# Optimization experiments

Measured on AMD Instinct MI355X. Metric: run time of the kernel, lower is better.

The kernel has to match this reference:

```python
import jax, jax.numpy as jnp
import numpy as np

EPS_NORM = 1e-12  # F.normalize eps
EPS_BN = 1e-5     # BatchNorm1d eps


def _gather_neighbors(tensor, index):
    # tensor: (bs, v, d), index: (bs, v, n) -> (bs, v, n, d)
    return jax.vmap(lambda t, i: t[i])(tensor, index)


def setup_inputs() -> dict:
    key = jax.random.key(0)
    ks = jax.random.split(key, 8)
    bs, v, n = 4, 4096, 32
    cin, cout = 128, 256
    stdv = float(np.sqrt(2.0 / cout))
    return {
        "neighbor_index": jax.random.randint(ks[0], (bs, v, n), 0, v),
        "vertices": jax.random.normal(ks[1], (bs, v, 3), dtype=jnp.float32),
        "feature_map": jax.random.normal(ks[2], (bs, v, cin - 1), dtype=jnp.float32),
        "directions": jax.random.uniform(ks[3], (4, cout), minval=-stdv, maxval=stdv, dtype=jnp.float32),
        "W": jax.random.normal(ks[4], (cout, cin), dtype=jnp.float32) / np.sqrt(cin),
        "b": jnp.zeros((cout,), jnp.float32),
        "gamma": jnp.ones((cout,), jnp.float32),
        "beta": jnp.zeros((cout,), jnp.float32),
    }


def reference(neighbor_index, vertices, feature_map, directions, W, b, gamma, beta):
    # --- direction-based weights theta: (bs, v, n, cout) ---
    neighbors = _gather_neighbors(vertices, neighbor_index)          # (bs,v,n,3)
    direc = neighbors - vertices[:, :, None, :]
    direc_norm = direc / jnp.maximum(
        jnp.linalg.norm(direc, axis=-1, keepdims=True), EPS_NORM)    # F.normalize
    dir_w = (direc_norm + 1.0) * 0.5                                  # (bs,v,n,3)
    sup_w = jnp.stack([directions[1] - directions[0],
                       directions[2] - directions[0],
                       directions[3] - directions[0]], axis=0)        # (3, cout)
    theta = jax.nn.relu(jnp.einsum('bvnk,kc->bvnc', dir_w, sup_w) + directions[0])

    # --- gathered features + L2 distance channel ---
    fs = _gather_neighbors(feature_map, neighbor_index)               # (bs,v,n,cin-1)
    fdist = jnp.sqrt(jnp.sum(fs * fs, axis=-1, keepdims=True))        # (bs,v,n,1)
    fs = jnp.concatenate([fs, fdist], axis=-1)                        # (bs,v,n,cin)

    # --- Linear -> BatchNorm1d (training stats) -> ReLU ---
    z = jnp.einsum('bvni,ci->bvnc', fs, W) + b                        # (bs,v,n,cout)
    mean = jnp.mean(z, axis=(0, 1, 2))
    var = jnp.mean(jnp.square(z - mean), axis=(0, 1, 2))              # biased var
    zn = (z - mean) * jax.lax.rsqrt(var + EPS_BN) * gamma + beta
    act = jax.nn.relu(zn) * theta

    # --- max-pool over neighbor dim ---
    return jnp.max(act, axis=2)                                       # (bs,v,cout)
```

## Files before the change

### kernel.cpp

```cpp
#include <hip/hip_runtime.h>

typedef unsigned short ushort_t;
typedef __attribute__((ext_vector_type(8))) short short8;
typedef __attribute__((ext_vector_type(4))) float floatx4;
typedef __attribute__((ext_vector_type(2))) float floatx2;

#define NN    32
#define CIN   128
#define COUT  256
#define NPTS  16384
#define NSAMP (NPTS * NN)
#define LDA   136
#define HB    128

__device__ __align__(16) ushort_t g_wb[COUT * CIN];
__device__ __align__(16) ushort_t g_y[(size_t)NPTS * COUT];
__device__ __align__(16) int      g_hp[HB * 4096];
__device__ __align__(16) float    g_sp[256 * 512];
__device__ __align__(16) float    g_consts[1536];

__device__ __forceinline__ float bf2f(ushort_t u) {
    return __uint_as_float(((unsigned int)u) << 16);
}
__device__ __forceinline__ ushort_t f2bf(float f) {
    unsigned int x = __float_as_uint(f);
    return (ushort_t)((x + 0x7FFFu + ((x >> 16) & 1u)) >> 16);
}
__device__ __forceinline__ int probe_f32(const void* verts, int lane) {
    float ax = fabsf(bf2f(((const ushort_t*)verts)[lane]));
    unsigned long long b = __ballot((ax > 1e-5f) && (ax < 32.0f));
    return (__popcll(b) >= 56) ? 0 : 1;
}

__global__ __launch_bounds__(256)
void hist_kernel(const int* __restrict__ nbr,
                 const void* __restrict__ Wg,
                 const void* __restrict__ verts) {
    __shared__ int h[4096];
    const int b   = blockIdx.x;
    const int tid = threadIdx.x;
    if (b < HB) {
        #pragma unroll
        for (int i = 0; i < 16; ++i) h[i * 256 + tid] = 0;
        __syncthreads();
        const int* src = nbr + (size_t)b * 4096;
        #pragma unroll
        for (int i = 0; i < 16; ++i) atomicAdd(&h[src[i * 256 + tid]], 1);
        __syncthreads();
        int* dst = g_hp + (size_t)b * 4096;
        #pragma unroll
        for (int i = 0; i < 16; ++i) dst[i * 256 + tid] = h[i * 256 + tid];
    } else {
        const int f32 = probe_f32(verts, tid & 63);
        int i = (b - HB) * 1024 + tid * 4;
        if (f32) {
            float4 v = ((const float4*)Wg)[i >> 2];
            g_wb[i] = f2bf(v.x); g_wb[i + 1] = f2bf(v.y);
            g_wb[i + 2] = f2bf(v.z); g_wb[i + 3] = f2bf(v.w);
        } else {
            *(uint2*)(g_wb + i) = *(const uint2*)((const ushort_t*)Wg + i);
        }
    }
}

__global__ __launch_bounds__(256, 2)
void ygemm_kernel(const void* __restrict__ fm, const void* __restrict__ verts) {
    __shared__ __align__(16) ushort_t At[64 * LDA];
    __shared__ float multS[64];

    const int tid  = threadIdx.x;
    const int r0   = blockIdx.x * 64;
    const int lane = tid & 63;
    const int f32  = probe_f32(verts, lane);

    if (tid < 64) {
        const int* hp = g_hp + (size_t)(r0 >> 12) * 32 * 4096 + (r0 & 4095) + tid;
        int s = 0;
        #pragma unroll
        for (int p2 = 0; p2 < 32; ++p2) s += hp[(size_t)p2 * 4096];
        multS[tid] = (float)s;
    }

    const int rl4 = tid >> 6;
    #pragma unroll 4
    for (int i = 0; i < 16; ++i) {
        const int rl = i * 4 + rl4;
        float f0, f1; ushort_t u0, u1;
        if (f32) {
            const float* src = (const float*)fm + (size_t)(r0 + rl) * 127;
            f0 = src[lane];
            f1 = (lane < 63) ? src[64 + lane] : 0.0f;
            u0 = f2bf(f0); u1 = f2bf(f1);
        } else {
            const ushort_t* src = (const ushort_t*)fm + (size_t)(r0 + rl) * 127;
            u0 = src[lane];
            u1 = (lane < 63) ? src[64 + lane] : (ushort_t)0;
            f0 = bf2f(u0); f1 = bf2f(u1);
        }
        float ss = f0 * f0 + f1 * f1;
        #pragma unroll
        for (int d = 1; d < 64; d <<= 1) ss += __shfl_xor(ss, d, 64);
        At[rl * LDA + lane]      = u0;
        At[rl * LDA + 64 + lane] = (lane < 63) ? u1 : f2bf(sqrtf(ss));
    }
    __syncthreads();

    const int w = tid >> 6;
    const int m = lane & 15;
    const int q = lane >> 4;

    floatx4 acc[4][4];
    #pragma unroll
    for (int rt = 0; rt < 4; ++rt)
        #pragma unroll
        for (int ct = 0; ct < 4; ++ct)
            acc[rt][ct] = (floatx4){0.0f, 0.0f, 0.0f, 0.0f};

    #pragma unroll
    for (int kk = 0; kk < 4; ++kk) {
        const int kof = kk * 32 + q * 8;
        short8 af[4];
        #pragma unroll
        for (int rt = 0; rt < 4; ++rt)
            af[rt] = *(const short8*)&At[(rt * 16 + m) * LDA + kof];
        short8 bfr[4];
        #pragma unroll
        for (int ct = 0; ct < 4; ++ct) {
            int ch = w * 64 + ct * 16 + m;
            bfr[ct] = *(const short8*)(g_wb + ch * CIN + kof);
        }
        #pragma unroll
        for (int rt = 0; rt < 4; ++rt)
            #pragma unroll
            for (int ct = 0; ct < 4; ++ct)
                acc[rt][ct] = __builtin_amdgcn_mfma_f32_16x16x32_bf16(
                    af[rt], bfr[ct], acc[rt][ct], 0, 0, 0);
    }

    #pragma unroll
    for (int ct = 0; ct < 4; ++ct) {
        const int ch = w * 64 + ct * 16 + m;
        float s = 0.0f, ss = 0.0f;
        #pragma unroll
        for (int rt = 0; rt < 4; ++rt)
            #pragma unroll
            for (int j = 0; j < 4; ++j) {
                int rloc = rt * 16 + q * 4 + j;
                ushort_t yb = f2bf(acc[rt][ct][j]);
                g_y[(size_t)(r0 + rloc) * COUT + ch] = yb;
                float yv = bf2f(yb);
                float wm = multS[rloc];
                s  += wm * yv;
                ss += wm * yv * yv;
            }
        s  += __shfl_xor(s, 16, 64);  s  += __shfl_xor(s, 32, 64);
        ss += __shfl_xor(ss, 16, 64); ss += __shfl_xor(ss, 32, 64);
        if (q == 0) {
            g_sp[(size_t)blockIdx.x * 512 + ch]       = s;
            g_sp[(size_t)blockIdx.x * 512 + 256 + ch] = ss;
        }
    }
}

__global__ void finalize_kernel(const void* __restrict__ gamma,
                                const void* __restrict__ beta,
                                const void* __restrict__ dirs,
                                const void* __restrict__ verts) {
    const int c   = threadIdx.x;
    const int f32 = probe_f32(verts, c & 63);

    float s = 0.0f, ss = 0.0f;
    #pragma unroll 8
    for (int p2 = 0; p2 < 256; ++p2) {
        s  += g_sp[(size_t)p2 * 512 + c];
        ss += g_sp[(size_t)p2 * 512 + 256 + c];
    }
    const float invN = 1.0f / (float)NSAMP;
    float mean = s * invN;
    float var  = fmaxf(ss * invN - mean * mean, 0.0f);
    float inv  = 1.0f / sqrtf(var + 1e-5f);
    float ga, be, d0, d1, d2, d3;
    if (f32) {
        ga = ((const float*)gamma)[c]; be = ((const float*)beta)[c];
        const float* dd = (const float*)dirs;
        d0 = dd[c]; d1 = dd[256 + c]; d2 = dd[512 + c]; d3 = dd[768 + c];
    } else {
        ga = bf2f(((const ushort_t*)gamma)[c]); be = bf2f(((const ushort_t*)beta)[c]);
        const ushort_t* dd = (const ushort_t*)dirs;
        d0 = bf2f(dd[c]); d1 = bf2f(dd[256 + c]);
        d2 = bf2f(dd[512 + c]); d3 = bf2f(dd[768 + c]);
    }
    float scale = ga * inv;
    g_consts[c]        = scale;
    g_consts[256 + c]  = be - mean * scale;
    g_consts[512 + c]  = d0;
    g_consts[768 + c]  = d1 - d0;
    g_consts[1024 + c] = d2 - d0;
    g_consts[1280 + c] = d3 - d0;
}

__global__ __launch_bounds__(256, 4)
void epi_kernel(const int* __restrict__ nbr,
                const void* __restrict__ verts,
                void* __restrict__ out) {
    __shared__ float4 dws[4][NN];

    const int tid  = threadIdx.x;
    const int lane = tid & 63;
    const int bid  = blockIdx.x;
    const int p0   = (((bid & 7) << 9) | (bid >> 3)) << 2;
    const int f32  = probe_f32(verts, lane);

    if (tid < 128) {
        const int pt = tid >> 5, j = tid & 31;
        const int p  = p0 + pt;
        int gv = ((p >> 12) << 12) + nbr[(size_t)p * NN + j];
        float sx, sy, sz, nx, ny, nz;
        if (f32) {
            const float* vv = (const float*)verts;
            sx = vv[p * 3]; sy = vv[p * 3 + 1]; sz = vv[p * 3 + 2];
            nx = vv[gv * 3]; ny = vv[gv * 3 + 1]; nz = vv[gv * 3 + 2];
        } else {
            const ushort_t* vv = (const ushort_t*)verts;
            sx = bf2f(vv[p * 3]); sy = bf2f(vv[p * 3 + 1]); sz = bf2f(vv[p * 3 + 2]);
            nx = bf2f(vv[gv * 3]); ny = bf2f(vv[gv * 3 + 1]); nz = bf2f(vv[gv * 3 + 2]);
        }
        float dx = nx - sx, dy = ny - sy, dz = nz - sz;
        float nrm = sqrtf(dx * dx + dy * dy + dz * dz);
        float inv = 1.0f / fmaxf(nrm, 1e-12f);
        dws[pt][j] = make_float4((dx * inv + 1.0f) * 0.5f,
                                 (dy * inv + 1.0f) * 0.5f,
                                 (dz * inv + 1.0f) * 0.5f,
                                 __int_as_float(gv));
    }
    __syncthreads();

    const int w  = tid >> 6;
    const int p  = p0 + w;
    const int c4 = lane * 4;
    const floatx4 zero = {0.0f, 0.0f, 0.0f, 0.0f};
    const floatx4 sc = *(const floatx4*)&g_consts[c4];
    const floatx4 sh = *(const floatx4*)&g_consts[256 + c4];
    const floatx4 d0 = *(const floatx4*)&g_consts[512 + c4];
    const floatx4 s0 = *(const floatx4*)&g_consts[768 + c4];
    const floatx4 s1 = *(const floatx4*)&g_consts[1024 + c4];
    const floatx4 s2 = *(const floatx4*)&g_consts[1280 + c4];

    const float4* dwp = dws[w];
    floatx4 vmA = zero, vmB = zero;

    for (int j0 = 0; j0 < NN; j0 += 4) {
        float4 dw[4]; uint2 u[4];
        #pragma unroll
        for (int jj = 0; jj < 4; ++jj) {
            dw[jj] = dwp[j0 + jj];
            int row = __float_as_int(dw[jj].w);
            u[jj] = *(const uint2*)(g_y + ((size_t)row << 8) + c4);
        }
        #pragma unroll
        for (int jj = 0; jj < 4; ++jj) {
            floatx4 y;
            y.x = __uint_as_float(u[jj].x << 16);
            y.y = __uint_as_float(u[jj].x & 0xFFFF0000u);
            y.z = __uint_as_float(u[jj].y << 16);
            y.w = __uint_as_float(u[jj].y & 0xFFFF0000u);
            floatx4 th = d0 + s0 * dw[jj].x + s1 * dw[jj].y + s2 * dw[jj].z;
            th = __builtin_elementwise_max(th, zero);
            floatx4 zt = (y * sc + sh) * th;
            if (jj & 1) vmB = __builtin_elementwise_max(vmB, zt);
            else        vmA = __builtin_elementwise_max(vmA, zt);
        }
    }
    floatx4 vm = __builtin_elementwise_max(vmA, vmB);

    size_t ofs = (size_t)p * COUT + c4;
    if (f32) {
        *(floatx4*)((float*)out + ofs) = vm;
    } else {
        uint2 ou;
        ou.x = ((unsigned int)f2bf(vm.y) << 16) | (unsigned int)f2bf(vm.x);
        ou.y = ((unsigned int)f2bf(vm.w) << 16) | (unsigned int)f2bf(vm.z);
        *(uint2*)((ushort_t*)out + ofs) = ou;
    }
}

extern "C" void kernel_launch(void* const* d_in, const int* in_sizes, int n_in,
                              void* d_out, int out_size, void* d_ws, size_t ws_size,
                              hipStream_t stream) {
    const int* nbr    = (const int*)d_in[0];
    const void* verts = d_in[1];
    const void* fm    = d_in[2];
    const void* dirs  = d_in[3];
    const void* Wg    = d_in[4];
    const void* gamma = d_in[6];
    const void* beta  = d_in[7];
    (void)d_ws; (void)ws_size; (void)in_sizes; (void)n_in; (void)out_size;

    hist_kernel<<<dim3(HB + 32), dim3(256), 0, stream>>>(nbr, Wg, verts);
    ygemm_kernel<<<dim3(NPTS / 64), dim3(256), 0, stream>>>(fm, verts);
    finalize_kernel<<<dim3(1), dim3(256), 0, stream>>>(gamma, beta, dirs, verts);
    epi_kernel<<<dim3(NPTS / 4), dim3(256), 0, stream>>>(nbr, verts, d_out);
}
```

Before: 141.0 us.

## Use per-wave readlane broadcasts and 8-deep load pipeline in epilogue

Each wave now computes its own point's neighbor direction weights in registers, lanes 0-31 holding one neighbor each, and broadcasts them with readlane. This removes the shared-memory staging and the block barrier. The gather of bf16 rows from the intermediate buffer is software-pipelined eight loads deep instead of four, and launch bounds rise to five blocks per SM. Each wave does the direction computation redundantly in its upper 32 lanes, and the deeper prefetch raises register pressure against the higher occupancy target.

```diff
diff --git a/kernel.cpp b/kernel.cpp
--- a/kernel.cpp
+++ b/kernel.cpp
@@ -30,6 +30,9 @@
     float ax = fabsf(bf2f(((const ushort_t*)verts)[lane]));
     unsigned long long b = __ballot((ax > 1e-5f) && (ax < 32.0f));
     return (__popcll(b) >= 56) ? 0 : 1;
+}
+__device__ __forceinline__ float lanebcast(float v, int jj) {
+    return __uint_as_float((unsigned)__builtin_amdgcn_readlane(__float_as_int(v), jj));
 }
 
 __global__ __launch_bounds__(256)
@@ -199,22 +202,22 @@
     g_consts[1280 + c] = d3 - d0;
 }
 
-__global__ __launch_bounds__(256, 4)
+__global__ __launch_bounds__(256, 5)
 void epi_kernel(const int* __restrict__ nbr,
                 const void* __restrict__ verts,
                 void* __restrict__ out) {
-    __shared__ float4 dws[4][NN];
-
     const int tid  = threadIdx.x;
     const int lane = tid & 63;
     const int bid  = blockIdx.x;
     const int p0   = (((bid & 7) << 9) | (bid >> 3)) << 2;
+    const int p    = p0 + (tid >> 6);
     const int f32  = probe_f32(verts, lane);
-
-    if (tid < 128) {
-        const int pt = tid >> 5, j = tid & 31;
-        const int p  = p0 + pt;
-        int gv = ((p >> 12) << 12) + nbr[(size_t)p * NN + j];
+    const int j    = lane & 31;
+
+    int   gv;
+    float wx, wy, wz;
+    {
+        gv = ((p >> 12) << 12) + nbr[(size_t)p * NN + j];
         float sx, sy, sz, nx, ny, nz;
         if (f32) {
             const float* vv = (const float*)verts;
@@ -228,15 +231,11 @@
         float dx = nx - sx, dy = ny - sy, dz = nz - sz;
         float nrm = sqrtf(dx * dx + dy * dy + dz * dz);
         float inv = 1.0f / fmaxf(nrm, 1e-12f);
-        dws[pt][j] = make_float4((dx * inv + 1.0f) * 0.5f,
-                                 (dy * inv + 1.0f) * 0.5f,
-                                 (dz * inv + 1.0f) * 0.5f,
-                                 __int_as_float(gv));
-    }
-    __syncthreads();
-
-    const int w  = tid >> 6;
-    const int p  = p0 + w;
+        wx = (dx * inv + 1.0f) * 0.5f;
+        wy = (dy * inv + 1.0f) * 0.5f;
+        wz = (dz * inv + 1.0f) * 0.5f;
+    }
+
     const int c4 = lane * 4;
     const floatx4 zero = {0.0f, 0.0f, 0.0f, 0.0f};
     const floatx4 sc = *(const floatx4*)&g_consts[c4];
@@ -246,29 +245,37 @@
     const floatx4 s1 = *(const floatx4*)&g_consts[1024 + c4];
     const floatx4 s2 = *(const floatx4*)&g_consts[1280 + c4];
 
-    const float4* dwp = dws[w];
     floatx4 vmA = zero, vmB = zero;
-
-    for (int j0 = 0; j0 < NN; j0 += 4) {
-        float4 dw[4]; uint2 u[4];
-        #pragma unroll
-        for (int jj = 0; jj < 4; ++jj) {
-            dw[jj] = dwp[j0 + jj];
-            int row = __float_as_int(dw[jj].w);
-            u[jj] = *(const uint2*)(g_y + ((size_t)row << 8) + c4);
-        }
-        #pragma unroll
-        for (int jj = 0; jj < 4; ++jj) {
+    uint2 u[8];
+
+    #pragma unroll
+    for (int k = 0; k < 8; ++k) {
+        int r = __builtin_amdgcn_readlane(gv, k);
+        u[k] = *(const uint2*)(g_y + ((size_t)(unsigned)r << 8) + c4);
+    }
+    #pragma unroll
+    for (int g = 0; g < 4; ++g) {
+        #pragma unroll
+        for (int k = 0; k < 8; ++k) {
+            const int jj = g * 8 + k;
+            const uint2 uk = u[k];
+            if (g < 3) {
+                int r = __builtin_amdgcn_readlane(gv, jj + 8);
+                u[k] = *(const uint2*)(g_y + ((size_t)(unsigned)r << 8) + c4);
+            }
+            float wxs = lanebcast(wx, jj);
+            float wys = lanebcast(wy, jj);
+            float wzs = lanebcast(wz, jj);
             floatx4 y;
-            y.x = __uint_as_float(u[jj].x << 16);
-            y.y = __uint_as_float(u[jj].x & 0xFFFF0000u);
-            y.z = __uint_as_float(u[jj].y << 16);
-            y.w = __uint_as_float(u[jj].y & 0xFFFF0000u);
-            floatx4 th = d0 + s0 * dw[jj].x + s1 * dw[jj].y + s2 * dw[jj].z;
+            y.x = __uint_as_float(uk.x << 16);
+            y.y = __uint_as_float(uk.x & 0xFFFF0000u);
+            y.z = __uint_as_float(uk.y << 16);
+            y.w = __uint_as_float(uk.y & 0xFFFF0000u);
+            floatx4 th = d0 + s0 * wxs + s1 * wys + s2 * wzs;
             th = __builtin_elementwise_max(th, zero);
             floatx4 zt = (y * sc + sh) * th;
-            if (jj & 1) vmB = __builtin_elementwise_max(vmB, zt);
-            else        vmA = __builtin_elementwise_max(vmA, zt);
+            if (k & 1) vmB = __builtin_elementwise_max(vmB, zt);
+            else       vmA = __builtin_elementwise_max(vmA, zt);
         }
     }
     floatx4 vm = __builtin_elementwise_max(vmA, vmB);
```

Result: no change. 140.5 us (-0.3%).
